# Kernel tuning notes

Hardware: AMD Instinct MI355X
Metric: run time of the kernel (lower is better)

## Reference

```python
import jax, jax.numpy as jnp
import numpy as np

B, L, H, E = 2, 2048, 16, 64  # S == L (causal self-attention), D == E


def setup_inputs() -> dict:
    key = jax.random.key(0)
    kq, kk, kv, ks = jax.random.split(key, 4)
    queries = jax.random.normal(kq, (B, L, H, E), dtype=jnp.float32)
    keys = jax.random.normal(kk, (B, L, H, E), dtype=jnp.float32)
    values = jax.random.normal(kv, (B, L, H, E), dtype=jnp.float32)
    # TriangularCausalMask: True above the diagonal -> masked out
    attn_mask = jnp.broadcast_to(
        jnp.triu(jnp.ones((L, L), dtype=bool), k=1)[None, None], (B, 1, L, L)
    )
    init_score = jax.random.uniform(ks, (B, L, L), dtype=jnp.float32)
    return {
        "queries": queries,
        "keys": keys,
        "values": values,
        "attn_mask": attn_mask,
        "init_score": init_score,
    }


def reference(queries, keys, values, attn_mask, init_score):
    # queries: [B,L,H,E], keys: [B,S,H,E], values: [B,S,H,D]
    E_ = queries.shape[-1]
    scale = 1.0 / np.sqrt(E_).astype(np.float32)
    # scores: [B,H,L,S]
    scores = jnp.einsum('blhe,bshe->bhls', queries, keys)
    scores = jnp.where(attn_mask, -jnp.inf, scores)
    A = jax.nn.softmax(scale * scores, axis=-1)  # dropout p=0 -> identity
    # post-softmax bias, broadcast over heads
    A = A + 0.1 * init_score[:, None, :, :]
    # V: [B,L,H,D]
    V = jnp.einsum('bhls,bshd->blhd', A, values)
    return V
```

## Files before the change

### kernel.cpp

```cpp
#include <hip/hip_runtime.h>
#include <hip/hip_bf16.h>
#include <math.h>

#define BB 2
#define LL 2048
#define HH 16
#define EE 64
#define LOG2E 1.44269504089f

typedef __attribute__((ext_vector_type(8))) short short8;
typedef __attribute__((ext_vector_type(4))) float floatx4;
typedef unsigned int u32;

union S8 { short8 v; u32 u[4]; ushort4 q[2]; };

__device__ inline u32 pkbf(float lo, float hi) {
    union { __hip_bfloat162 h; u32 u; } c;
    c.h = __float22bfloat162_rn(make_float2(lo, hi));
    return c.u;
}

__device__ inline ushort4 cvt4(float4 v) {
    union { __hip_bfloat162 h; u32 u; } a, b;
    a.h = __float22bfloat162_rn(make_float2(v.x, v.y));
    b.h = __float22bfloat162_rn(make_float2(v.z, v.w));
    ushort4 r;
    r.x = (unsigned short)(a.u & 0xffffu);
    r.y = (unsigned short)(a.u >> 16);
    r.z = (unsigned short)(b.u & 0xffffu);
    r.w = (unsigned short)(b.u >> 16);
    return r;
}

__device__ inline short8 pack8(float4 a, float4 b) {
    S8 s; s.q[0] = cvt4(a); s.q[1] = cvt4(b); return s.v;
}

__device__ inline void async16(unsigned short* lds, const unsigned short* g) {
    __builtin_amdgcn_global_load_lds(
        (const __attribute__((address_space(1))) u32*)g,
        (__attribute__((address_space(3))) u32*)lds, 16, 0, 0);
}

__global__ __launch_bounds__(256) void prepass(
    const float* __restrict__ k, const float* __restrict__ v,
    const float* __restrict__ isc, unsigned short* __restrict__ kb,
    unsigned short* __restrict__ vt, unsigned short* __restrict__ isb)
{
    const int bid = blockIdx.x;
    const int t = threadIdx.x;
    if (bid < 1024) {
        #pragma unroll
        for (int it = 0; it < 2; ++it) {
            int idx = bid * 512 + it * 256 + t;
            const float4* src = (const float4*)k + idx * 2;
            float4 a = src[0], c = src[1];
            int e8 = idx & 7, h = (idx >> 3) & 15, l = (idx >> 7) & 2047, b = idx >> 18;
            *(short8*)&kb[(((b * 16 + h) * 2048 + l) * 64) + e8 * 8] = pack8(a, c);
        }
    } else if (bid < 2048) {
        __shared__ float Tf[64][69];
        const int vb = bid - 1024;
        const int st = vb & 31, h = (vb >> 5) & 15, b = vb >> 9;
        const int s0 = st * 64;
        #pragma unroll
        for (int i = 0; i < 4; ++i) {
            int r = i * 16 + (t >> 4), c = (t & 15) * 4;
            float4 val = *(const float4*)(v + (((b * LL + s0 + r) * HH + h) * EE) + c);
            *(float4*)&Tf[r][c] = val;
        }
        __syncthreads();
        #pragma unroll
        for (int i = 0; i < 2; ++i) {
            int slot = t + i * 256;
            int d = slot >> 3, s8 = (slot & 7) * 8;
            float4 lo = make_float4(Tf[s8 + 0][d], Tf[s8 + 1][d],
                                    Tf[s8 + 2][d], Tf[s8 + 3][d]);
            float4 hi = make_float4(Tf[s8 + 4][d], Tf[s8 + 5][d],
                                    Tf[s8 + 6][d], Tf[s8 + 7][d]);
            *(short8*)&vt[((b * 16 + h) * 64 + d) * 2048 + s0 + s8] = pack8(lo, hi);
        }
    } else {
        const int ib = bid - 2048;
        #pragma unroll
        for (int it = 0; it < 2; ++it) {
            int idx = ib * 512 + it * 256 + t;
            const float4* src = (const float4*)isc + idx * 2;
            float4 a = src[0], c = src[1];
            a.x *= 0.1f; a.y *= 0.1f; a.z *= 0.1f; a.w *= 0.1f;
            c.x *= 0.1f; c.y *= 0.1f; c.z *= 0.1f; c.w *= 0.1f;
            ((short8*)isb)[idx] = pack8(a, c);
        }
    }
}

template <int MODE>
__device__ __forceinline__ void tile_step(
    const unsigned short* __restrict__ Ks, const unsigned short* __restrict__ Vs,
    const short8 qf[2], const short8 isf[2], const short8 ones,
    floatx4 o_attn[4], floatx4 o_bias[4], floatx4& o_sum,
    int s0, int mbase, int wave, int lq, int ln, int lnl,
    int alo, int ahi, bool hisel)
{
    u32 pk[4][2];
    if (MODE < 2) {
        #pragma unroll
        for (int sb = 0; sb < 4; ++sb) {
            if (MODE == 1 && wave < sb) { pk[sb][0] = 0; pk[sb][1] = 0; continue; }
            short8 kf0 = *(const short8*)&Ks[(sb * 16 + ln) * 64 + ((lq ^ lnl) << 3)];
            short8 kf1 = *(const short8*)&Ks[(sb * 16 + ln) * 64 + (((4 + lq) ^ lnl) << 3)];
            floatx4 sa = {0.f, 0.f, 0.f, 0.f};
            __builtin_amdgcn_s_setprio(1);
            sa = __builtin_amdgcn_mfma_f32_16x16x32_bf16(kf0, qf[0], sa, 0, 0, 0);
            sa = __builtin_amdgcn_mfma_f32_16x16x32_bf16(kf1, qf[1], sa, 0, 0, 0);
            __builtin_amdgcn_s_setprio(0);
            float pv[4];
            #pragma unroll
            for (int r = 0; r < 4; ++r) {
                float t = sa[r];
                if (MODE == 1 && (s0 + sb * 16 + lq * 4 + r) > (mbase + ln)) t = -INFINITY;
                pv[r] = exp2f(t);
            }
            pk[sb][0] = pkbf(pv[0], pv[1]);
            pk[sb][1] = pkbf(pv[2], pv[3]);
        }
    }
    #pragma unroll
    for (int kk = 0; kk < 2; ++kk) {
        short8 vf[4];
        #pragma unroll
        for (int db = 0; db < 4; ++db)
            vf[db] = *(const short8*)&Vs[(db * 16 + ln) * 64 + (((kk * 4 + lq) ^ lnl) << 3)];
        short8 af = isf[kk];
        __builtin_amdgcn_s_setprio(1);
        #pragma unroll
        for (int db = 0; db < 4; ++db)
            o_bias[db] = __builtin_amdgcn_mfma_f32_16x16x32_bf16(af, vf[db], o_bias[db], 0, 0, 0);
        __builtin_amdgcn_s_setprio(0);
        if (MODE < 2) {
            S8 pf;
            u32 a0 = (u32)__builtin_amdgcn_ds_bpermute(alo, (int)pk[kk * 2][0]);
            u32 b0 = (u32)__builtin_amdgcn_ds_bpermute(alo, (int)pk[kk * 2 + 1][0]);
            pf.u[0] = hisel ? b0 : a0;
            u32 a1 = (u32)__builtin_amdgcn_ds_bpermute(alo, (int)pk[kk * 2][1]);
            u32 b1 = (u32)__builtin_amdgcn_ds_bpermute(alo, (int)pk[kk * 2 + 1][1]);
            pf.u[1] = hisel ? b1 : a1;
            u32 a2 = (u32)__builtin_amdgcn_ds_bpermute(ahi, (int)pk[kk * 2][0]);
            u32 b2 = (u32)__builtin_amdgcn_ds_bpermute(ahi, (int)pk[kk * 2 + 1][0]);
            pf.u[2] = hisel ? b2 : a2;
            u32 a3 = (u32)__builtin_amdgcn_ds_bpermute(ahi, (int)pk[kk * 2][1]);
            u32 b3 = (u32)__builtin_amdgcn_ds_bpermute(ahi, (int)pk[kk * 2 + 1][1]);
            pf.u[3] = hisel ? b3 : a3;
            __builtin_amdgcn_s_setprio(1);
            o_sum = __builtin_amdgcn_mfma_f32_16x16x32_bf16(pf.v, ones, o_sum, 0, 0, 0);
            #pragma unroll
            for (int db = 0; db < 4; ++db)
                o_attn[db] = __builtin_amdgcn_mfma_f32_16x16x32_bf16(pf.v, vf[db], o_attn[db], 0, 0, 0);
            __builtin_amdgcn_s_setprio(0);
        }
    }
}

__global__ __launch_bounds__(256, 4) void fused10(
    const float* __restrict__ q, const unsigned short* __restrict__ kb,
    const unsigned short* __restrict__ vt, const unsigned short* __restrict__ isb,
    float* __restrict__ out)
{
    __shared__ unsigned short Ks[2][64 * 64];
    __shared__ unsigned short Vs[2][64 * 64];

    const int tid = threadIdx.x, lane = tid & 63, wave = tid >> 6;
    const int lq = lane >> 4, ln = lane & 15, lnl = ln & 7;

    const int bid = blockIdx.x;
    const int h = bid & 15, b = (bid >> 4) & 1, g = bid >> 5;
    int qt;
    if (g < 8) qt = 31 - g;
    else if (g < 16) qt = g;
    else if (g < 24) qt = 39 - g;
    else qt = g - 24;
    const int q0 = qt * 64;
    const int mbase = q0 + wave * 16;

    short8 qf[2];
    {
        const float sc = 0.125f * LOG2E;
        const float* qrow = q + (((long)(b * LL + mbase + ln)) * HH + h) * EE;
        #pragma unroll
        for (int kk = 0; kk < 2; ++kk) {
            float4 a = *(const float4*)(qrow + kk * 32 + lq * 8);
            float4 c = *(const float4*)(qrow + kk * 32 + lq * 8 + 4);
            a.x *= sc; a.y *= sc; a.z *= sc; a.w *= sc;
            c.x *= sc; c.y *= sc; c.z *= sc; c.w *= sc;
            qf[kk] = pack8(a, c);
        }
    }

    const unsigned short* kbh = kb + (long)(b * HH + h) * (LL * EE);
    const unsigned short* vth = vt + (long)(b * HH + h) * (EE * LL);

    floatx4 o_attn[4], o_bias[4];
    #pragma unroll
    for (int db = 0; db < 4; ++db) {
        o_attn[db] = (floatx4){0.f, 0.f, 0.f, 0.f};
        o_bias[db] = (floatx4){0.f, 0.f, 0.f, 0.f};
    }
    floatx4 o_sum = (floatx4){0.f, 0.f, 0.f, 0.f};
    const short8 ones = {(short)0x3F80, (short)0x3F80, (short)0x3F80, (short)0x3F80,
                         (short)0x3F80, (short)0x3F80, (short)0x3F80, (short)0x3F80};

    const int rr = lane >> 3, jl = lane & 7;
    const int swz = (jl ^ rr) * 8;
    const unsigned short* ksrc0 = kbh + (wave * 16 + rr) * 64 + swz;
    const unsigned short* ksrc1 = kbh + (wave * 16 + 8 + rr) * 64 + swz;
    const unsigned short* vsrc0 = vth + (wave * 16 + rr) * LL + swz;
    const unsigned short* vsrc1 = vth + (wave * 16 + 8 + rr) * LL + swz;

    const unsigned short* isrow =
        isb + (long)(b * LL + q0 + wave * 16 + ln) * LL + lq * 8;

    const int alo = (((lq & 1) * 2) * 16 + ln) * 4;
    const int ahi = (((lq & 1) * 2 + 1) * 16 + ln) * 4;
    const bool hisel = (lq >= 2);

    auto issue = [&](int j) {
        const int s0 = j * 64, bsel = j & 1;
        if (j <= qt) {
            async16(&Ks[bsel][(wave * 16) * 64], ksrc0 + s0 * 64);
            async16(&Ks[bsel][(wave * 16 + 8) * 64], ksrc1 + s0 * 64);
        }
        async16(&Vs[bsel][(wave * 16) * 64], vsrc0 + s0);
        async16(&Vs[bsel][(wave * 16 + 8) * 64], vsrc1 + s0);
    };

    short8 isf[2], isfn[2];
    auto ldnext = [&](int j, short8* dst) {
        int jc = j < 32 ? j : 31;
        dst[0] = *(const short8*)(isrow + jc * 64);
        dst[1] = *(const short8*)(isrow + jc * 64 + 32);
    };

    ldnext(0, isf);
    issue(0);
    for (int j = 0; j < qt; ++j) {
        __syncthreads();
        issue(j + 1);
        ldnext(j + 1, isfn);
        tile_step<0>(Ks[j & 1], Vs[j & 1], qf, isf, ones, o_attn, o_bias, o_sum,
                     j * 64, mbase, wave, lq, ln, lnl, alo, ahi, hisel);
        isf[0] = isfn[0]; isf[1] = isfn[1];
    }
    {
        __syncthreads();
        if (qt < 31) issue(qt + 1);
        ldnext(qt + 1, isfn);
        tile_step<1>(Ks[qt & 1], Vs[qt & 1], qf, isf, ones, o_attn, o_bias, o_sum,
                     q0, mbase, wave, lq, ln, lnl, alo, ahi, hisel);
        isf[0] = isfn[0]; isf[1] = isfn[1];
    }
    for (int j = qt + 1; j < 32; ++j) {
        __syncthreads();
        if (j < 31) issue(j + 1);
        ldnext(j + 1, isfn);
        tile_step<2>(Vs[j & 1], Vs[j & 1], qf, isf, ones, o_attn, o_bias, o_sum,
                     j * 64, mbase, wave, lq, ln, lnl, alo, ahi, hisel);
        isf[0] = isfn[0]; isf[1] = isfn[1];
    }

    #pragma unroll
    for (int r = 0; r < 4; ++r) {
        float inv = 1.0f / o_sum[r];
        int m = mbase + lq * 4 + r;
        float* ob = out + (((long)(b * LL + m)) * HH + h) * EE;
        #pragma unroll
        for (int db = 0; db < 4; ++db)
            ob[db * 16 + ln] = o_attn[db][r] * inv + o_bias[db][r];
    }
}

extern "C" void kernel_launch(void* const* d_in, const int* in_sizes, int n_in,
                              void* d_out, int out_size, void* d_ws, size_t ws_size,
                              hipStream_t stream) {
    (void)in_sizes; (void)n_in; (void)out_size; (void)ws_size;
    const float* q   = (const float*)d_in[0];
    const float* k   = (const float*)d_in[1];
    const float* v   = (const float*)d_in[2];
    const float* isc = (const float*)d_in[4];
    float* out = (float*)d_out;

    unsigned short* kb  = (unsigned short*)d_ws;
    unsigned short* vt  = (unsigned short*)((char*)d_ws + (8u << 20));
    unsigned short* isb = (unsigned short*)((char*)d_ws + (16u << 20));

    prepass<<<dim3(4096), dim3(256), 0, stream>>>(k, v, isc, kb, vt, isb);
    fused10<<<dim3(1024), dim3(256), 0, stream>>>(q, kb, vt, isb, out);
}
```

Measured before the change: 195.6 us.

## Software-pipeline QK of next tile with PV of previous tile using triple-buffered V

Splits the per-tile work into QK, exp/pack, and PV phases and skews them so the QK MFMAs for tile j are issued before the PV MFMAs of tile j-1, with the exp/pack done afterwards. The intent is to hide exp latency and MFMA dependency stalls behind independent matrix work. V shared memory grows to three buffers so the previous tile's V stays valid while the next one loads. The cost is extra LDS, more live registers (score accumulators plus packed probabilities across iterations), and a single loop with runtime mode branches instead of three specialised loops.

```diff
diff --git a/kernel.cpp b/kernel.cpp
--- a/kernel.cpp
+++ b/kernel.cpp
@@ -95,49 +95,63 @@
 }
 
 template <int MODE>
-__device__ __forceinline__ void tile_step(
-    const unsigned short* __restrict__ Ks, const unsigned short* __restrict__ Vs,
-    const short8 qf[2], const short8 isf[2], const short8 ones,
+__device__ __forceinline__ void qk_phase(
+    const unsigned short* __restrict__ Ks, const short8 qf[2], floatx4 sa[4],
+    int wave, int lq, int ln, int lnl)
+{
+    #pragma unroll
+    for (int sb = 0; sb < 4; ++sb) {
+        if (MODE == 1 && wave < sb) continue;
+        short8 kf0 = *(const short8*)&Ks[(sb * 16 + ln) * 64 + ((lq ^ lnl) << 3)];
+        short8 kf1 = *(const short8*)&Ks[(sb * 16 + ln) * 64 + (((4 + lq) ^ lnl) << 3)];
+        floatx4 s = {0.f, 0.f, 0.f, 0.f};
+        __builtin_amdgcn_s_setprio(1);
+        s = __builtin_amdgcn_mfma_f32_16x16x32_bf16(kf0, qf[0], s, 0, 0, 0);
+        s = __builtin_amdgcn_mfma_f32_16x16x32_bf16(kf1, qf[1], s, 0, 0, 0);
+        __builtin_amdgcn_s_setprio(0);
+        sa[sb] = s;
+    }
+}
+
+template <int MODE>
+__device__ __forceinline__ void pack_phase(
+    const floatx4 sa[4], u32 pk[4][2], int s0, int mbase,
+    int wave, int lq, int ln)
+{
+    #pragma unroll
+    for (int sb = 0; sb < 4; ++sb) {
+        if (MODE == 1 && wave < sb) { pk[sb][0] = 0; pk[sb][1] = 0; continue; }
+        float pv[4];
+        #pragma unroll
+        for (int r = 0; r < 4; ++r) {
+            float t = sa[sb][r];
+            if (MODE == 1 && (s0 + sb * 16 + lq * 4 + r) > (mbase + ln)) t = -INFINITY;
+            pv[r] = exp2f(t);
+        }
+        pk[sb][0] = pkbf(pv[0], pv[1]);
+        pk[sb][1] = pkbf(pv[2], pv[3]);
+    }
+}
+
+template <bool ATT>
+__device__ __forceinline__ void pv_phase(
+    const unsigned short* __restrict__ Vs, const short8 isf[2],
+    const u32 pk[4][2], const short8 ones,
     floatx4 o_attn[4], floatx4 o_bias[4], floatx4& o_sum,
-    int s0, int mbase, int wave, int lq, int ln, int lnl,
-    int alo, int ahi, bool hisel)
-{
-    u32 pk[4][2];
-    if (MODE < 2) {
-        #pragma unroll
-        for (int sb = 0; sb < 4; ++sb) {
-            if (MODE == 1 && wave < sb) { pk[sb][0] = 0; pk[sb][1] = 0; continue; }
-            short8 kf0 = *(const short8*)&Ks[(sb * 16 + ln) * 64 + ((lq ^ lnl) << 3)];
-            short8 kf1 = *(const short8*)&Ks[(sb * 16 + ln) * 64 + (((4 + lq) ^ lnl) << 3)];
-            floatx4 sa = {0.f, 0.f, 0.f, 0.f};
-            __builtin_amdgcn_s_setprio(1);
-            sa = __builtin_amdgcn_mfma_f32_16x16x32_bf16(kf0, qf[0], sa, 0, 0, 0);
-            sa = __builtin_amdgcn_mfma_f32_16x16x32_bf16(kf1, qf[1], sa, 0, 0, 0);
-            __builtin_amdgcn_s_setprio(0);
-            float pv[4];
-            #pragma unroll
-            for (int r = 0; r < 4; ++r) {
-                float t = sa[r];
-                if (MODE == 1 && (s0 + sb * 16 + lq * 4 + r) > (mbase + ln)) t = -INFINITY;
-                pv[r] = exp2f(t);
-            }
-            pk[sb][0] = pkbf(pv[0], pv[1]);
-            pk[sb][1] = pkbf(pv[2], pv[3]);
-        }
-    }
+    int lq, int ln, int lnl, int alo, int ahi, bool hisel)
+{
     #pragma unroll
     for (int kk = 0; kk < 2; ++kk) {
         short8 vf[4];
         #pragma unroll
         for (int db = 0; db < 4; ++db)
             vf[db] = *(const short8*)&Vs[(db * 16 + ln) * 64 + (((kk * 4 + lq) ^ lnl) << 3)];
-        short8 af = isf[kk];
         __builtin_amdgcn_s_setprio(1);
         #pragma unroll
         for (int db = 0; db < 4; ++db)
-            o_bias[db] = __builtin_amdgcn_mfma_f32_16x16x32_bf16(af, vf[db], o_bias[db], 0, 0, 0);
+            o_bias[db] = __builtin_amdgcn_mfma_f32_16x16x32_bf16(isf[kk], vf[db], o_bias[db], 0, 0, 0);
         __builtin_amdgcn_s_setprio(0);
-        if (MODE < 2) {
+        if (ATT) {
             S8 pf;
             u32 a0 = (u32)__builtin_amdgcn_ds_bpermute(alo, (int)pk[kk * 2][0]);
             u32 b0 = (u32)__builtin_amdgcn_ds_bpermute(alo, (int)pk[kk * 2 + 1][0]);
@@ -161,13 +175,13 @@
     }
 }
 
-__global__ __launch_bounds__(256, 4) void fused10(
+__global__ __launch_bounds__(256, 4) void fused13(
     const float* __restrict__ q, const unsigned short* __restrict__ kb,
     const unsigned short* __restrict__ vt, const unsigned short* __restrict__ isb,
     float* __restrict__ out)
 {
     __shared__ unsigned short Ks[2][64 * 64];
-    __shared__ unsigned short Vs[2][64 * 64];
+    __shared__ unsigned short Vs[3][64 * 64];
 
     const int tid = threadIdx.x, lane = tid & 63, wave = tid >> 6;
     const int lq = lane >> 4, ln = lane & 15, lnl = ln & 7;
@@ -223,49 +237,52 @@
     const int ahi = (((lq & 1) * 2 + 1) * 16 + ln) * 4;
     const bool hisel = (lq >= 2);
 
-    auto issue = [&](int j) {
-        const int s0 = j * 64, bsel = j & 1;
-        if (j <= qt) {
-            async16(&Ks[bsel][(wave * 16) * 64], ksrc0 + s0 * 64);
-            async16(&Ks[bsel][(wave * 16 + 8) * 64], ksrc1 + s0 * 64);
-        }
-        async16(&Vs[bsel][(wave * 16) * 64], vsrc0 + s0);
-        async16(&Vs[bsel][(wave * 16 + 8) * 64], vsrc1 + s0);
+    auto issue = [&](int t) {
+        const int s0 = t * 64;
+        if (t <= qt) {
+            async16(&Ks[t & 1][(wave * 16) * 64], ksrc0 + s0 * 64);
+            async16(&Ks[t & 1][(wave * 16 + 8) * 64], ksrc1 + s0 * 64);
+        }
+        const int v3 = t % 3;
+        async16(&Vs[v3][(wave * 16) * 64], vsrc0 + s0);
+        async16(&Vs[v3][(wave * 16 + 8) * 64], vsrc1 + s0);
     };
 
-    short8 isf[2], isfn[2];
+    short8 isfC[2], isfP[2];
     auto ldnext = [&](int j, short8* dst) {
         int jc = j < 32 ? j : 31;
         dst[0] = *(const short8*)(isrow + jc * 64);
         dst[1] = *(const short8*)(isrow + jc * 64 + 32);
     };
 
-    ldnext(0, isf);
+    ldnext(0, isfC);
     issue(0);
-    for (int j = 0; j < qt; ++j) {
-        __syncthreads();
-        issue(j + 1);
-        ldnext(j + 1, isfn);
-        tile_step<0>(Ks[j & 1], Vs[j & 1], qf, isf, ones, o_attn, o_bias, o_sum,
-                     j * 64, mbase, wave, lq, ln, lnl, alo, ahi, hisel);
-        isf[0] = isfn[0]; isf[1] = isfn[1];
-    }
-    {
-        __syncthreads();
-        if (qt < 31) issue(qt + 1);
-        ldnext(qt + 1, isfn);
-        tile_step<1>(Ks[qt & 1], Vs[qt & 1], qf, isf, ones, o_attn, o_bias, o_sum,
-                     q0, mbase, wave, lq, ln, lnl, alo, ahi, hisel);
-        isf[0] = isfn[0]; isf[1] = isfn[1];
-    }
-    for (int j = qt + 1; j < 32; ++j) {
+
+    u32 pkP[4][2];
+    int pm = 2;
+    for (int j = 0; j < 32; ++j) {
         __syncthreads();
         if (j < 31) issue(j + 1);
-        ldnext(j + 1, isfn);
-        tile_step<2>(Vs[j & 1], Vs[j & 1], qf, isf, ones, o_attn, o_bias, o_sum,
-                     j * 64, mbase, wave, lq, ln, lnl, alo, ahi, hisel);
-        isf[0] = isfn[0]; isf[1] = isfn[1];
-    }
+        const int m = (j < qt) ? 0 : ((j == qt) ? 1 : 2);
+        floatx4 sa[4];
+        if (m == 0)      qk_phase<0>(Ks[j & 1], qf, sa, wave, lq, ln, lnl);
+        else if (m == 1) qk_phase<1>(Ks[j & 1], qf, sa, wave, lq, ln, lnl);
+        if (j > 0) {
+            if (pm < 2) pv_phase<true >(Vs[(j - 1) % 3], isfP, pkP, ones,
+                                        o_attn, o_bias, o_sum, lq, ln, lnl, alo, ahi, hisel);
+            else        pv_phase<false>(Vs[(j - 1) % 3], isfP, pkP, ones,
+                                        o_attn, o_bias, o_sum, lq, ln, lnl, alo, ahi, hisel);
+        }
+        if (m == 0)      pack_phase<0>(sa, pkP, j * 64, mbase, wave, lq, ln);
+        else if (m == 1) pack_phase<1>(sa, pkP, j * 64, mbase, wave, lq, ln);
+        isfP[0] = isfC[0]; isfP[1] = isfC[1];
+        ldnext(j + 1, isfC);
+        pm = m;
+    }
+    if (pm < 2) pv_phase<true >(Vs[31 % 3], isfP, pkP, ones,
+                                o_attn, o_bias, o_sum, lq, ln, lnl, alo, ahi, hisel);
+    else        pv_phase<false>(Vs[31 % 3], isfP, pkP, ones,
+                                o_attn, o_bias, o_sum, lq, ln, lnl, alo, ahi, hisel);
 
     #pragma unroll
     for (int r = 0; r < 4; ++r) {
@@ -293,5 +310,5 @@
     unsigned short* isb = (unsigned short*)((char*)d_ws + (16u << 20));
 
     prepass<<<dim3(4096), dim3(256), 0, stream>>>(k, v, isc, kb, vt, isb);
-    fused10<<<dim3(1024), dim3(256), 0, stream>>>(q, kb, vt, isb, out);
-}
+    fused13<<<dim3(1024), dim3(256), 0, stream>>>(q, kb, vt, isb, out);
+}
```

After: 228.8 us. 1.17x slower.
